# Optimization experiments

Measured on AMD Instinct MI355X. Metric: run time of the kernel, lower is better.

## Reference

```python
import jax, jax.numpy as jnp
import numpy as np

N_EXPERTS = 64
LN_EPS = 1e-5


def _layer_norm(x, gamma, beta, eps=LN_EPS):
    mu = jnp.mean(x, axis=-1, keepdims=True)
    var = jnp.mean(jnp.square(x - mu), axis=-1, keepdims=True)
    return (x - mu) * jax.lax.rsqrt(var + eps) * gamma + beta


def setup_inputs() -> dict:
    key = jax.random.key(0)
    ks = jax.random.split(key, 4)
    B, T, D, Ff = 2, 1024, 512, 2048
    x = jax.random.normal(ks[0], (B, T, D), dtype=jnp.float32)
    hex_weights = jax.random.uniform(ks[1], (B, T, N_EXPERTS), dtype=jnp.float32)
    W_in = jax.random.normal(ks[2], (N_EXPERTS, Ff, D), dtype=jnp.float32) * (D ** -0.5)
    b_in = jnp.zeros((N_EXPERTS, Ff), dtype=jnp.float32)
    W_out = jax.random.normal(ks[3], (N_EXPERTS, D, Ff), dtype=jnp.float32) * (Ff ** -0.5)
    b_out = jnp.zeros((N_EXPERTS, D), dtype=jnp.float32)
    ln_gamma = jnp.ones((D,), dtype=jnp.float32)
    ln_beta = jnp.zeros((D,), dtype=jnp.float32)
    return {"x": x, "hex_weights": hex_weights, "W_in": W_in, "b_in": b_in,
            "W_out": W_out, "b_out": b_out, "ln_gamma": ln_gamma,
            "ln_beta": ln_beta, "top_k": 4}


def reference(x, hex_weights, W_in, b_in, W_out, b_out, ln_gamma, ln_beta, top_k):
    B, T, D = x.shape
    N = B * T
    x_n = _layer_norm(x, ln_gamma, ln_beta)

    # top-k routing; renormalize the selected weights (matches torch topk + sum-norm)
    top_w, top_idx = jax.lax.top_k(hex_weights, top_k)          # (B,T,k)
    top_w = top_w / (jnp.sum(top_w, axis=-1, keepdims=True) + 1e-8)

    x_flat = x_n.reshape(N, D)
    # Scatter the k normalized weights into a dense (N, 64) routing matrix.
    # Non-selected experts get weight 0, so a dense per-expert sweep computes
    # EXACTLY the same combined output as the per-token gather in the original.
    w_full = jnp.zeros((N, N_EXPERTS), dtype=x.dtype)
    w_full = w_full.at[jnp.arange(N)[:, None], top_idx.reshape(N, top_k)].set(
        top_w.reshape(N, top_k))

    def body(acc, e):
        W_in_e, b_in_e, W_out_e, b_out_e, we = e  # we: (N,)
        h = jax.nn.silu(x_flat @ W_in_e.T + b_in_e)            # (N, d_ff)
        acc = acc + we[:, None] * (h @ W_out_e.T + b_out_e)    # (N, D)
        return acc, None

    acc, _ = jax.lax.scan(body, jnp.zeros_like(x_flat),
                          (W_in, b_in, W_out, b_out, w_full.T))
    return acc.reshape(B, T, D)
```

## Files before the change

### kernel.cpp

```cpp
#include <hip/hip_runtime.h>

#define NTOK 2048
#define DD   512
#define FFD  2048
#define NE   64
#define KSEL 4
#define NPAIR (NTOK*KSEL)
#define BM 192
#define NT 128
#define HROWS (NPAIR + 256)

typedef short s16x8 __attribute__((ext_vector_type(8)));
typedef float f32x4 __attribute__((ext_vector_type(4)));

typedef const __attribute__((address_space(1))) char* gptr_t;
typedef __attribute__((address_space(3))) char* lptr_t;

static __device__ __forceinline__ unsigned short f2bf(float f) {
    unsigned int u = __builtin_bit_cast(unsigned int, f);
    u += 0x7FFFu + ((u >> 16) & 1u);
    return (unsigned short)(u >> 16);
}

static __device__ __forceinline__ s16x8 cvt8(float4 a, float4 b) {
    s16x8 r;
    r[0] = (short)f2bf(a.x); r[1] = (short)f2bf(a.y);
    r[2] = (short)f2bf(a.z); r[3] = (short)f2bf(a.w);
    r[4] = (short)f2bf(b.x); r[5] = (short)f2bf(b.y);
    r[6] = (short)f2bf(b.z); r[7] = (short)f2bf(b.w);
    return r;
}

__global__ __launch_bounds__(256) void k_ln_route(
    const float* __restrict__ x, const float* __restrict__ hw,
    const float* __restrict__ gamma, const float* __restrict__ beta,
    unsigned short* __restrict__ xn_bf, int* __restrict__ counts,
    int* __restrict__ tok_e, float* __restrict__ tok_w)
{
    const int t = blockIdx.x;
    const int tid = threadIdx.x;
    const float* xr = x + (size_t)t * DD;
    float v0 = xr[tid];
    float v1 = xr[tid + 256];
    float s = v0 + v1, s2 = v0*v0 + v1*v1;
    #pragma unroll
    for (int off = 32; off > 0; off >>= 1) {
        s  += __shfl_down(s, off);
        s2 += __shfl_down(s2, off);
    }
    __shared__ float rsum[4], rsum2[4];
    __shared__ float smu, srs;
    const int wid = tid >> 6, lane = tid & 63;
    if (lane == 0) { rsum[wid] = s; rsum2[wid] = s2; }
    __syncthreads();
    if (tid == 0) {
        float a = 0.f, b = 0.f;
        for (int i = 0; i < 4; ++i) { a += rsum[i]; b += rsum2[i]; }
        float mu  = a * (1.f / DD);
        float var = b * (1.f / DD) - mu * mu;
        smu = mu; srs = rsqrtf(var + 1e-5f);
    }
    __syncthreads();
    const float mu = smu, rstd = srs;
    xn_bf[(size_t)t*DD + tid]       = f2bf((v0 - mu) * rstd * gamma[tid]       + beta[tid]);
    xn_bf[(size_t)t*DD + tid + 256] = f2bf((v1 - mu) * rstd * gamma[tid + 256] + beta[tid + 256]);

    if (tid < 64) {
        float v = hw[(size_t)t*NE + tid];
        int   sel[KSEL]; float sw[KSEL];
        #pragma unroll
        for (int j = 0; j < KSEL; ++j) {
            float m = v; int mi = tid;
            #pragma unroll
            for (int off = 32; off > 0; off >>= 1) {
                float ov = __shfl_xor(m, off);
                int   oi = __shfl_xor(mi, off);
                if (ov > m || (ov == m && oi < mi)) { m = ov; mi = oi; }
            }
            if (tid == mi) v = -1e30f;
            sel[j] = mi; sw[j] = m;
        }
        if (tid == 0) {
            float ssum = sw[0] + sw[1] + sw[2] + sw[3];
            float inv = 1.f / (ssum + 1e-8f);
            #pragma unroll
            for (int j = 0; j < KSEL; ++j) {
                tok_e[t*KSEL + j] = sel[j];
                tok_w[t*KSEL + j] = sw[j] * inv;
                atomicAdd(&counts[sel[j]], 1);
            }
        }
    }
}

__global__ void k_scan(const int* __restrict__ counts, int* __restrict__ offs,
                       int* __restrict__ cursor, int* __restrict__ tile_e,
                       int* __restrict__ tile_r, int* __restrict__ ntiles)
{
    __shared__ int sc[NE], stc[NE];
    const int tid = threadIdx.x;
    sc[tid] = counts[tid];
    __syncthreads();
    int off = 0;
    for (int i = 0; i < tid; ++i) off += sc[i];
    offs[tid] = off; cursor[tid] = off;
    if (tid == NE-1) offs[NE] = off + sc[NE-1];
    int tc = (sc[tid] + BM - 1) / BM;
    stc[tid] = tc;
    __syncthreads();
    int toff = 0;
    for (int i = 0; i < tid; ++i) toff += stc[i];
    for (int j = 0; j < tc; ++j) { tile_e[toff + j] = tid; tile_r[toff + j] = off + j*BM; }
    if (tid == NE-1) *ntiles = toff + tc;
}

__global__ __launch_bounds__(256) void k_scatter(
    const int* __restrict__ tok_e, const float* __restrict__ tok_w,
    int* __restrict__ cursor, int* __restrict__ pair_tok,
    float* __restrict__ pair_w, int* __restrict__ inv)
{
    int i = blockIdx.x * 256 + threadIdx.x;
    if (i >= NPAIR) return;
    int t = i >> 2;
    int e = tok_e[i];
    int slot = atomicAdd(&cursor[e], 1);
    pair_tok[slot] = t;
    pair_w[slot] = tok_w[i];
    inv[i] = slot;
}

template<int KD, bool IS_IN, int NYG>
__global__ __launch_bounds__(256, 3) void k_moe_gemm(
    const unsigned short* __restrict__ Abf,
    const float* __restrict__ W, const float* __restrict__ bias,
    const int* __restrict__ tile_e, const int* __restrict__ tile_r,
    const int* __restrict__ ntiles, const int* __restrict__ offs,
    const int* __restrict__ pr_tok, const float* __restrict__ pr_w,
    unsigned short* __restrict__ Hout, float* __restrict__ Pout)
{
    constexpr int NK = KD / 32;
    const int ti = blockIdx.x / NYG;
    const int yg = blockIdx.x % NYG;
    if (ti >= *ntiles) return;
    const int e    = tile_e[ti];
    const int row0 = tile_r[ti];
    const int rend = offs[e + 1];
    const int n0   = yg * 64;
    const int NOUT = IS_IN ? FFD : DD;

    __shared__ __align__(16) unsigned short As[3 * BM * 32];
    __shared__ __align__(16) unsigned short Bs[2 * 64 * 32];

    const int tid  = threadIdx.x;
    const int lane = tid & 63, wave = tid >> 6;
    const int lr = lane & 15, lk = lane >> 4;

    const char* asrc[3];
    #pragma unroll
    for (int i = 0; i < 3; ++i) {
        int seg  = wave * 3 + i;
        int r    = seg * 16 + (lane >> 2);
        int cg   = (lane & 3) ^ ((lane >> 2) & 3);
        int grow = row0 + r;
        size_t rowbase;
        if (IS_IN) {
            int tok = (grow < rend) ? pr_tok[grow] : pr_tok[row0];
            rowbase = (size_t)tok * (KD * 2);
        } else {
            rowbase = (size_t)grow * (KD * 2);
        }
        asrc[i] = (const char*)Abf + rowbase + (size_t)cg * 16;
    }

    const float* wptr = W + (size_t)e * NOUT * KD + (size_t)(n0 + (tid >> 2)) * KD + (tid & 3) * 8;
    char* bdst0 = (char*)Bs + (tid >> 2) * 64 + (((tid & 3) ^ ((tid >> 2) & 3)) << 4);

    f32x4 acc[3][4];
    #pragma unroll
    for (int m = 0; m < 3; ++m)
        #pragma unroll
        for (int n = 0; n < 4; ++n)
            acc[m][n] = (f32x4){0.f, 0.f, 0.f, 0.f};

    float4 waA0, waA1, waB0, waB1;

    waA0 = *(const float4*)(wptr);
    waA1 = *(const float4*)(wptr + 4);
    asm volatile("s_waitcnt vmcnt(0)" ::: "memory");
    __builtin_amdgcn_sched_barrier(0);
    *(s16x8*)bdst0 = cvt8(waA0, waA1);
    #pragma unroll
    for (int i = 0; i < 3; ++i)
        __builtin_amdgcn_global_load_lds((gptr_t)asrc[i],
            (lptr_t)((char*)As + (wave * 3 + i) * 1024), 16, 0, 0);
    __builtin_amdgcn_sched_barrier(0);
    waB0 = *(const float4*)(wptr + 32);
    waB1 = *(const float4*)(wptr + 36);
    __builtin_amdgcn_sched_barrier(0);
    #pragma unroll
    for (int i = 0; i < 3; ++i)
        __builtin_amdgcn_global_load_lds((gptr_t)(asrc[i] + 64),
            (lptr_t)((char*)As + 12288 + (wave * 3 + i) * 1024), 16, 0, 0);

    int ab0 = 0, ab1 = 1, ab2 = 2;

#define GEMM_STEP(KT, WUSE0, WUSE1, WISS0, WISS1)                                        \
    {                                                                                    \
        if ((KT) == NK - 1) asm volatile("s_waitcnt vmcnt(0) lgkmcnt(0)" ::: "memory");  \
        else                asm volatile("s_waitcnt vmcnt(5) lgkmcnt(0)" ::: "memory");  \
        __builtin_amdgcn_s_barrier();                                                    \
        __builtin_amdgcn_sched_barrier(0);                                               \
        if ((KT) + 2 < NK) {                                                             \
            WISS0 = *(const float4*)(wptr + ((KT) + 2) * 32);                            \
            WISS1 = *(const float4*)(wptr + ((KT) + 2) * 32 + 4);                        \
        }                                                                                \
        __builtin_amdgcn_sched_barrier(0);                                               \
        if ((KT) + 2 < NK) {                                                             \
            _Pragma("unroll")                                                            \
            for (int i = 0; i < 3; ++i)                                                  \
                __builtin_amdgcn_global_load_lds(                                        \
                    (gptr_t)(asrc[i] + (size_t)((KT) + 2) * 64),                         \
                    (lptr_t)((char*)As + ab2 * 12288 + (wave * 3 + i) * 1024),           \
                    16, 0, 0);                                                           \
        }                                                                                \
        __builtin_amdgcn_sched_barrier(0);                                               \
        {                                                                                \
            const char* Ab = (const char*)As + ab0 * 12288;                              \
            const char* Bb = (const char*)Bs + ((KT) & 1) * 4096;                        \
            const int sw = ((lk ^ (lr & 3)) << 4);                                       \
            s16x8 af[3], bfr[4];                                                         \
            _Pragma("unroll")                                                            \
            for (int m = 0; m < 3; ++m)                                                  \
                af[m] = *(const s16x8*)(Ab + (wave * 48 + m * 16 + lr) * 64 + sw);       \
            _Pragma("unroll")                                                            \
            for (int n = 0; n < 4; ++n)                                                  \
                bfr[n] = *(const s16x8*)(Bb + (n * 16 + lr) * 64 + sw);                  \
            _Pragma("unroll")                                                            \
            for (int m = 0; m < 3; ++m)                                                  \
                _Pragma("unroll")                                                        \
                for (int n = 0; n < 4; ++n)                                              \
                    acc[m][n] = __builtin_amdgcn_mfma_f32_16x16x32_bf16(                 \
                        af[m], bfr[n], acc[m][n], 0, 0, 0);                              \
        }                                                                                \
        __builtin_amdgcn_sched_barrier(0);                                               \
        if ((KT) + 1 < NK) {                                                             \
            if ((KT) + 2 < NK) asm volatile("s_waitcnt vmcnt(8)" ::: "memory");          \
            else               asm volatile("s_waitcnt vmcnt(3)" ::: "memory");          \
            __builtin_amdgcn_sched_barrier(0);                                           \
            *(s16x8*)(bdst0 + (((KT) + 1) & 1) * 4096) = cvt8(WUSE0, WUSE1);             \
        }                                                                                \
        int tmp_ = ab0; ab0 = ab1; ab1 = ab2; ab2 = tmp_;                                \
    }

    for (int kt = 0; kt < NK; kt += 2) {
        GEMM_STEP(kt,     waB0, waB1, waA0, waA1);
        GEMM_STEP(kt + 1, waA0, waA1, waB0, waB1);
    }
#undef GEMM_STEP

    #pragma unroll
    for (int m = 0; m < 3; ++m) {
        #pragma unroll
        for (int r = 0; r < 4; ++r) {
            int row = row0 + wave * 48 + m * 16 + lk * 4 + r;
            if (row < rend) {
                if (IS_IN) {
                    #pragma unroll
                    for (int n = 0; n < 4; ++n) {
                        int f = n0 + n * 16 + lr;
                        float v = acc[m][n][r] + bias[e * FFD + f];
                        v = v / (1.f + __expf(-v));
                        Hout[(size_t)row * FFD + f] = f2bf(v);
                    }
                } else {
                    float pw = pr_w[row];
                    #pragma unroll
                    for (int n = 0; n < 4; ++n) {
                        int d = n0 + n * 16 + lr;
                        Pout[(size_t)row * DD + d] = (acc[m][n][r] + bias[e * DD + d]) * pw;
                    }
                }
            }
        }
    }
}

__global__ __launch_bounds__(128) void k_combine(
    const float* __restrict__ pout, const int* __restrict__ inv,
    float* __restrict__ out)
{
    const int t = blockIdx.x;
    const int tid = threadIdx.x;
    const float4* p0 = (const float4*)(pout + (size_t)inv[t*4+0]*DD);
    const float4* p1 = (const float4*)(pout + (size_t)inv[t*4+1]*DD);
    const float4* p2 = (const float4*)(pout + (size_t)inv[t*4+2]*DD);
    const float4* p3 = (const float4*)(pout + (size_t)inv[t*4+3]*DD);
    float4 a = p0[tid], b = p1[tid], c = p2[tid], d = p3[tid];
    float4 r;
    r.x = a.x + b.x + c.x + d.x;
    r.y = a.y + b.y + c.y + d.y;
    r.z = a.z + b.z + c.z + d.z;
    r.w = a.w + b.w + c.w + d.w;
    ((float4*)(out + (size_t)t*DD))[tid] = r;
}

extern "C" void kernel_launch(void* const* d_in, const int* in_sizes, int n_in,
                              void* d_out, int out_size, void* d_ws, size_t ws_size,
                              hipStream_t stream)
{
    const float* x     = (const float*)d_in[0];
    const float* hw    = (const float*)d_in[1];
    const float* Win   = (const float*)d_in[2];
    const float* bin   = (const float*)d_in[3];
    const float* Wout  = (const float*)d_in[4];
    const float* bout  = (const float*)d_in[5];
    const float* gamma = (const float*)d_in[6];
    const float* beta  = (const float*)d_in[7];
    float* out = (float*)d_out;

    char* ws = (char*)d_ws;
    size_t o = 0;
    unsigned short* xn_bf = (unsigned short*)(ws + o); o += (size_t)NTOK * DD * 2;
    unsigned short* H     = (unsigned short*)(ws + o); o += (size_t)HROWS * FFD * 2;
    float* pout   = (float*)(ws + o); o += (size_t)NPAIR * DD * 4;
    int*   counts = (int*)(ws + o);   o += 256;
    int*   offs   = (int*)(ws + o);   o += 512;
    int*   cursor = (int*)(ws + o);   o += 256;
    int*   tok_e  = (int*)(ws + o);   o += (size_t)NPAIR * 4;
    float* tok_w  = (float*)(ws + o); o += (size_t)NPAIR * 4;
    int*   inv    = (int*)(ws + o);   o += (size_t)NPAIR * 4;
    int*   pr_tok = (int*)(ws + o);   o += (size_t)NPAIR * 4;
    float* pr_w   = (float*)(ws + o); o += (size_t)NPAIR * 4;
    int*   tile_e = (int*)(ws + o);   o += 512;
    int*   tile_r = (int*)(ws + o);   o += 512;
    int*   ntiles = (int*)(ws + o);   o += 256;
    (void)ws_size; (void)in_sizes; (void)n_in; (void)out_size;

    hipMemsetAsync(counts, 0, 256, stream);
    k_ln_route<<<dim3(NTOK), dim3(256), 0, stream>>>(x, hw, gamma, beta, xn_bf, counts, tok_e, tok_w);
    k_scan<<<dim3(1), dim3(64), 0, stream>>>(counts, offs, cursor, tile_e, tile_r, ntiles);
    k_scatter<<<dim3(NPAIR/256), dim3(256), 0, stream>>>(tok_e, tok_w, cursor, pr_tok, pr_w, inv);

    k_moe_gemm<DD, true, FFD/64><<<dim3(NT * (FFD/64)), dim3(256), 0, stream>>>(
        xn_bf, Win, bin, tile_e, tile_r, ntiles, offs, pr_tok, pr_w, H, nullptr);
    k_moe_gemm<FFD, false, DD/64><<<dim3(NT * (DD/64)), dim3(256), 0, stream>>>(
        H, Wout, bout, tile_e, tile_r, ntiles, offs, pr_tok, pr_w, nullptr, pout);

    k_combine<<<dim3(NTOK), dim3(128), 0, stream>>>(pout, inv, out);
}
```

Measured before the change: 261.5 us.

## Load expert weights directly into registers per wave, dropping LDS B staging and barriers

The grouped MoE GEMM no longer stages the fp32 weight tile through shared memory. Each wave now loads its own 4×16-column slice of weights into registers and converts it to bf16 MFMA operands in place. Because each wave only reads the A rows it loaded itself, the per-step s_barrier and LDS write/read of B are removed, which cuts synchronisation and LDS traffic. In exchange, each wave issues four times as many global weight loads with a less coalesced pattern, and the double-buffered fp32 registers raise register pressure.

```diff
diff --git a/kernel.cpp b/kernel.cpp
--- a/kernel.cpp
+++ b/kernel.cpp
@@ -149,7 +149,6 @@
     const int NOUT = IS_IN ? FFD : DD;
 
     __shared__ __align__(16) unsigned short As[3 * BM * 32];
-    __shared__ __align__(16) unsigned short Bs[2 * 64 * 32];
 
     const int tid  = threadIdx.x;
     const int lane = tid & 63, wave = tid >> 6;
@@ -172,8 +171,7 @@
         asrc[i] = (const char*)Abf + rowbase + (size_t)cg * 16;
     }
 
-    const float* wptr = W + (size_t)e * NOUT * KD + (size_t)(n0 + (tid >> 2)) * KD + (tid & 3) * 8;
-    char* bdst0 = (char*)Bs + (tid >> 2) * 64 + (((tid & 3) ^ ((tid >> 2) & 3)) << 4);
+    const float* wf = W + (size_t)e * NOUT * KD + (size_t)(n0 + lr) * KD + lk * 8;
 
     f32x4 acc[3][4];
     #pragma unroll
@@ -182,21 +180,22 @@
         for (int n = 0; n < 4; ++n)
             acc[m][n] = (f32x4){0.f, 0.f, 0.f, 0.f};
 
-    float4 waA0, waA1, waB0, waB1;
-
-    waA0 = *(const float4*)(wptr);
-    waA1 = *(const float4*)(wptr + 4);
-    asm volatile("s_waitcnt vmcnt(0)" ::: "memory");
-    __builtin_amdgcn_sched_barrier(0);
-    *(s16x8*)bdst0 = cvt8(waA0, waA1);
+    float4 wA[8], wB[8];
+
+    #pragma unroll
+    for (int n = 0; n < 4; ++n) {
+        wA[2*n]   = *(const float4*)(wf + (size_t)n * 16 * KD);
+        wA[2*n+1] = *(const float4*)(wf + (size_t)n * 16 * KD + 4);
+    }
     #pragma unroll
     for (int i = 0; i < 3; ++i)
         __builtin_amdgcn_global_load_lds((gptr_t)asrc[i],
             (lptr_t)((char*)As + (wave * 3 + i) * 1024), 16, 0, 0);
-    __builtin_amdgcn_sched_barrier(0);
-    waB0 = *(const float4*)(wptr + 32);
-    waB1 = *(const float4*)(wptr + 36);
-    __builtin_amdgcn_sched_barrier(0);
+    #pragma unroll
+    for (int n = 0; n < 4; ++n) {
+        wB[2*n]   = *(const float4*)(wf + (size_t)n * 16 * KD + 32);
+        wB[2*n+1] = *(const float4*)(wf + (size_t)n * 16 * KD + 36);
+    }
     #pragma unroll
     for (int i = 0; i < 3; ++i)
         __builtin_amdgcn_global_load_lds((gptr_t)(asrc[i] + 64),
@@ -204,18 +203,22 @@
 
     int ab0 = 0, ab1 = 1, ab2 = 2;
 
-#define GEMM_STEP(KT, WUSE0, WUSE1, WISS0, WISS1)                                        \
+#define GEMM_STEP(KT, WSET)                                                              \
     {                                                                                    \
-        if ((KT) == NK - 1) asm volatile("s_waitcnt vmcnt(0) lgkmcnt(0)" ::: "memory");  \
-        else                asm volatile("s_waitcnt vmcnt(5) lgkmcnt(0)" ::: "memory");  \
-        __builtin_amdgcn_s_barrier();                                                    \
+        if ((KT) == NK - 1) asm volatile("s_waitcnt vmcnt(0)" ::: "memory");             \
+        else                asm volatile("s_waitcnt vmcnt(11)" ::: "memory");            \
+        __builtin_amdgcn_sched_barrier(0);                                               \
+        s16x8 bfr[4];                                                                    \
+        _Pragma("unroll")                                                                \
+        for (int n = 0; n < 4; ++n)                                                      \
+            bfr[n] = cvt8(WSET[2*n], WSET[2*n+1]);                                       \
         __builtin_amdgcn_sched_barrier(0);                                               \
         if ((KT) + 2 < NK) {                                                             \
-            WISS0 = *(const float4*)(wptr + ((KT) + 2) * 32);                            \
-            WISS1 = *(const float4*)(wptr + ((KT) + 2) * 32 + 4);                        \
-        }                                                                                \
-        __builtin_amdgcn_sched_barrier(0);                                               \
-        if ((KT) + 2 < NK) {                                                             \
+            _Pragma("unroll")                                                            \
+            for (int n = 0; n < 4; ++n) {                                                \
+                WSET[2*n]   = *(const float4*)(wf + (size_t)n*16*KD + ((KT)+2)*32);      \
+                WSET[2*n+1] = *(const float4*)(wf + (size_t)n*16*KD + ((KT)+2)*32 + 4);  \
+            }                                                                            \
             _Pragma("unroll")                                                            \
             for (int i = 0; i < 3; ++i)                                                  \
                 __builtin_amdgcn_global_load_lds(                                        \
@@ -226,15 +229,11 @@
         __builtin_amdgcn_sched_barrier(0);                                               \
         {                                                                                \
             const char* Ab = (const char*)As + ab0 * 12288;                              \
-            const char* Bb = (const char*)Bs + ((KT) & 1) * 4096;                        \
-            const int sw = ((lk ^ (lr & 3)) << 4);                                       \
-            s16x8 af[3], bfr[4];                                                         \
+            s16x8 af[3];                                                                 \
             _Pragma("unroll")                                                            \
             for (int m = 0; m < 3; ++m)                                                  \
-                af[m] = *(const s16x8*)(Ab + (wave * 48 + m * 16 + lr) * 64 + sw);       \
-            _Pragma("unroll")                                                            \
-            for (int n = 0; n < 4; ++n)                                                  \
-                bfr[n] = *(const s16x8*)(Bb + (n * 16 + lr) * 64 + sw);                  \
+                af[m] = *(const s16x8*)(Ab + (wave*48 + m*16 + lr) * 64                  \
+                                           + ((lk ^ (lr & 3)) << 4));                    \
             _Pragma("unroll")                                                            \
             for (int m = 0; m < 3; ++m)                                                  \
                 _Pragma("unroll")                                                        \
@@ -242,19 +241,12 @@
                     acc[m][n] = __builtin_amdgcn_mfma_f32_16x16x32_bf16(                 \
                         af[m], bfr[n], acc[m][n], 0, 0, 0);                              \
         }                                                                                \
-        __builtin_amdgcn_sched_barrier(0);                                               \
-        if ((KT) + 1 < NK) {                                                             \
-            if ((KT) + 2 < NK) asm volatile("s_waitcnt vmcnt(8)" ::: "memory");          \
-            else               asm volatile("s_waitcnt vmcnt(3)" ::: "memory");          \
-            __builtin_amdgcn_sched_barrier(0);                                           \
-            *(s16x8*)(bdst0 + (((KT) + 1) & 1) * 4096) = cvt8(WUSE0, WUSE1);             \
-        }                                                                                \
         int tmp_ = ab0; ab0 = ab1; ab1 = ab2; ab2 = tmp_;                                \
     }
 
     for (int kt = 0; kt < NK; kt += 2) {
-        GEMM_STEP(kt,     waB0, waB1, waA0, waA1);
-        GEMM_STEP(kt + 1, waA0, waA1, waB0, waB1);
+        GEMM_STEP(kt,     wA);
+        GEMM_STEP(kt + 1, wB);
     }
 #undef GEMM_STEP
 
```

New measurement: 532.8 us. 104% more time.
